# Kernel tuning notes

Hardware: AMD Instinct MI355X
Metric: run time of the kernel (lower is better)

The kernel has to match this reference:

```python
import jax, jax.numpy as jnp
import numpy as np

B, SX, SL, D, H = 4, 4096, 256, 1024, 16
DH = D // H
LN_EPS = 1e-5
RMS_EPS = 1e-8


def layernorm(x, g, b):
    mu = jnp.mean(x, axis=-1, keepdims=True)
    var = jnp.mean(jnp.square(x - mu), axis=-1, keepdims=True)
    return (x - mu) * jax.lax.rsqrt(var + LN_EPS) * g + b


def rmsnorm(x, gamma):
    # torch: norm = ||x||_2 * dim^-0.5 ; x / clamp(norm, eps) * gamma
    norm = jnp.sqrt(jnp.sum(jnp.square(x), axis=-1, keepdims=True)) * (DH ** -0.5)
    return x / jnp.maximum(norm, RMS_EPS) * gamma


def setup_inputs() -> dict:
    key = jax.random.key(0)
    ks = jax.random.split(key, 6)
    s = 0.02
    return {
        "x": jax.random.normal(ks[0], (B, SX, D), jnp.float32),
        "latents": jax.random.normal(ks[1], (B, SL, D), jnp.float32),
        "mask_x": jnp.ones((B, SX), jnp.float32),
        "mask_latent": jnp.ones((B, SL), jnp.float32),
        "ln_x_g": jnp.ones((D,), jnp.float32),
        "ln_x_b": jnp.zeros((D,), jnp.float32),
        "ln_l_g": jnp.ones((D,), jnp.float32),
        "ln_l_b": jnp.zeros((D,), jnp.float32),
        "Wq": jax.random.normal(ks[2], (D, D), jnp.float32) * s,
        "Wkv": jax.random.normal(ks[3], (D, 2 * D), jnp.float32) * s,
        "qk_gamma": jnp.ones((DH,), jnp.float32),
        "Wo": jax.random.normal(ks[4], (D, D), jnp.float32) * s,
    }


def reference(x, latents, mask_x, mask_latent, ln_x_g, ln_x_b, ln_l_g, ln_l_b, Wq, Wkv, qk_gamma, Wo):
    xn = layernorm(x, ln_x_g, ln_x_b)                       # [B,SX,D]
    ln = layernorm(latents, ln_l_g, ln_l_b)                 # [B,SL,D]

    q = (ln @ Wq).reshape(B, SL, H, DH).transpose(0, 2, 1, 3)      # [B,H,SL,DH]
    kv_in = jnp.concatenate([xn, ln], axis=1)                      # [B,SX+SL,D]
    kv = kv_in @ Wkv
    Skv = SX + SL
    k = kv[..., :D].reshape(B, Skv, H, DH).transpose(0, 2, 1, 3)   # [B,H,Skv,DH]
    v = kv[..., D:].reshape(B, Skv, H, DH).transpose(0, 2, 1, 3)

    # NOTE: original code applies query_norm to BOTH q and k (faithful to source)
    q = rmsnorm(q, qk_gamma)
    k = rmsnorm(k, qk_gamma)

    scores = jnp.einsum("bhqd,bhkd->bhqk", q, k) / np.sqrt(DH)     # [B,H,SL,Skv]

    kv_mask = jnp.concatenate([mask_x, mask_latent], axis=1)       # [B,Skv]
    mask = kv_mask[:, None, :] * mask_latent[:, :, None]           # [B,SL,Skv]
    add_mask = (1.0 - mask)[:, None, :, :] * jnp.finfo(scores.dtype).min
    attn = jax.nn.softmax(scores + add_mask, axis=-1)

    y = jnp.einsum("bhqk,bhkd->bhqd", attn, v)                     # [B,H,SL,DH]
    y = y.transpose(0, 2, 1, 3).reshape(B, SL, D)
    return y @ Wo
```

## Files before the change

### kernel.cpp

```cpp
#include <hip/hip_runtime.h>

#define NB   4
#define SXX  4096
#define SLL  256
#define DD   1024
#define HH   16
#define DHH  64
#define SKV  4352
#define MKV  17408
#define NSPLIT 8

typedef __attribute__((ext_vector_type(8))) short bfrag;
typedef __attribute__((ext_vector_type(4))) float facc;

__device__ __forceinline__ unsigned short f2bf(float f){
  unsigned u = __builtin_bit_cast(unsigned, f);
  u = (u + 0x7fffu + ((u >> 16) & 1u)) >> 16;
  return (unsigned short)u;
}
__device__ __forceinline__ float bf2f(unsigned short h){
  unsigned u = ((unsigned)h) << 16;
  return __builtin_bit_cast(float, u);
}

#define GLOAD_LDS16(g, lds) __builtin_amdgcn_global_load_lds( \
    (const __attribute__((address_space(1))) unsigned int*)(const void*)(g), \
    (__attribute__((address_space(3))) unsigned int*)(void*)(lds), 16, 0, 0)

__global__ void wtrans3(const float* __restrict__ Wq, const float* __restrict__ Wkv,
                        const float* __restrict__ Wo, unsigned short* __restrict__ wqt,
                        unsigned short* __restrict__ wkvt, unsigned short* __restrict__ wot){
  __shared__ float t[32][33];
  int z = blockIdx.z;
  const float* in; unsigned short* out; int N;
  if (z == 0){ in = Wq;  out = wqt;  N = DD;   }
  else if (z == 1){ in = Wkv; out = wkvt; N = 2*DD; }
  else { in = Wo;  out = wot;  N = DD;   }
  int n0 = blockIdx.x * 32, k0 = blockIdx.y * 32;
  if (n0 >= N) return;
  int tx = threadIdx.x, ty = threadIdx.y;
  #pragma unroll
  for (int i = 0; i < 4; i++)
    t[ty + 8*i][tx] = in[(size_t)(k0 + ty + 8*i) * N + n0 + tx];
  __syncthreads();
  #pragma unroll
  for (int i = 0; i < 4; i++)
    out[(size_t)(n0 + ty + 8*i) * DD + k0 + tx] = f2bf(t[tx][ty + 8*i]);
}

__global__ void lnorm(const float* __restrict__ src, const float* __restrict__ g,
                      const float* __restrict__ bt, unsigned short* __restrict__ kvin,
                      unsigned short* __restrict__ dst2, int seq, int off){
  int row = blockIdx.x;
  int b = row / seq, s = row - b*seq;
  int t = threadIdx.x;
  const float4* rp = (const float4*)(src + (size_t)row * DD);
  float4 v = rp[t];
  float sum = v.x + v.y + v.z + v.w;
  float sq  = v.x*v.x + v.y*v.y + v.z*v.z + v.w*v.w;
  #pragma unroll
  for (int o = 32; o > 0; o >>= 1){ sum += __shfl_down(sum, o); sq += __shfl_down(sq, o); }
  __shared__ float ls[8];
  int w = t >> 6, l = t & 63;
  if (l == 0){ ls[w] = sum; ls[4 + w] = sq; }
  __syncthreads();
  sum = ls[0] + ls[1] + ls[2] + ls[3];
  sq  = ls[4] + ls[5] + ls[6] + ls[7];
  float mu  = sum * (1.f/DD);
  float var = sq * (1.f/DD) - mu*mu;
  float rs  = rsqrtf(var + 1e-5f);
  float4 gv = ((const float4*)g)[t];
  float4 bv = ((const float4*)bt)[t];
  ushort4 o4;
  o4.x = f2bf((v.x - mu)*rs*gv.x + bv.x);
  o4.y = f2bf((v.y - mu)*rs*gv.y + bv.y);
  o4.z = f2bf((v.z - mu)*rs*gv.z + bv.z);
  o4.w = f2bf((v.w - mu)*rs*gv.w + bv.w);
  *(ushort4*)(kvin + (size_t)(b*SKV + off + s) * DD + t*4) = o4;
  if (dst2) *(ushort4*)(dst2 + (size_t)row * DD + t*4) = o4;
}

__global__ __launch_bounds__(256) void gemm64(const unsigned short* __restrict__ A,
    const unsigned short* __restrict__ Bt, int M, int N, int K, float* __restrict__ outF){
  __shared__ unsigned short lA[64][72];
  __shared__ unsigned short lB[64][72];
  int n0 = blockIdx.x * 64, m0 = blockIdx.y * 64;
  int t = threadIdx.x, w = t >> 6, l = t & 63;
  int wr = (w >> 1) * 32, wc = (w & 1) * 32;
  int lr = l & 15, kq = (l >> 4) * 8;
  facc acc00 = (facc)0.f, acc01 = (facc)0.f, acc10 = (facc)0.f, acc11 = (facc)0.f;
  for (int k0 = 0; k0 < K; k0 += 64){
    #pragma unroll
    for (int cc = 0; cc < 2; cc++){
      int ch = t + cc*256;
      int row = ch >> 3, cg = (ch & 7) * 8;
      *(bfrag*)&lA[row][cg] = *(const bfrag*)&A[(size_t)(m0 + row) * K + k0 + cg];
      *(bfrag*)&lB[row][cg] = *(const bfrag*)&Bt[(size_t)(n0 + row) * K + k0 + cg];
    }
    __syncthreads();
    #pragma unroll
    for (int ks = 0; ks < 2; ks++){
      bfrag a0 = *(const bfrag*)&lA[wr + lr][ks*32 + kq];
      bfrag a1 = *(const bfrag*)&lA[wr + 16 + lr][ks*32 + kq];
      bfrag b0 = *(const bfrag*)&lB[wc + lr][ks*32 + kq];
      bfrag b1 = *(const bfrag*)&lB[wc + 16 + lr][ks*32 + kq];
      acc00 = __builtin_amdgcn_mfma_f32_16x16x32_bf16(a0, b0, acc00, 0, 0, 0);
      acc01 = __builtin_amdgcn_mfma_f32_16x16x32_bf16(a0, b1, acc01, 0, 0, 0);
      acc10 = __builtin_amdgcn_mfma_f32_16x16x32_bf16(a1, b0, acc10, 0, 0, 0);
      acc11 = __builtin_amdgcn_mfma_f32_16x16x32_bf16(a1, b1, acc11, 0, 0, 0);
    }
    __syncthreads();
  }
  int rl = (l >> 4) * 4, cl = l & 15;
  facc accs[2][2] = {{acc00, acc01},{acc10, acc11}};
  #pragma unroll
  for (int mt = 0; mt < 2; mt++)
  #pragma unroll
  for (int nt = 0; nt < 2; nt++)
  #pragma unroll
  for (int j = 0; j < 4; j++){
    int r = m0 + wr + mt*16 + rl + j;
    int c = n0 + wc + nt*16 + cl;
    outF[(size_t)r * N + c] = accs[mt][nt][j];
  }
}

__global__ __launch_bounds__(256) void gemm_q(const unsigned short* __restrict__ A,
    const unsigned short* __restrict__ Bt, const float* __restrict__ gamma,
    unsigned short* __restrict__ qn){
  __shared__ char smemb[18432];
  unsigned short* lA = (unsigned short*)smemb;
  unsigned short* lB = lA + 64*72;
  float* Cf = (float*)smemb;
  int h = blockIdx.x, n0 = h * 64, m0 = blockIdx.y * 64;
  int t = threadIdx.x, w = t >> 6, l = t & 63;
  int wr = (w >> 1) * 32, wc = (w & 1) * 32;
  int lr = l & 15, kq = (l >> 4) * 8;
  facc acc00 = (facc)0.f, acc01 = (facc)0.f, acc10 = (facc)0.f, acc11 = (facc)0.f;
  for (int k0 = 0; k0 < 1024; k0 += 64){
    #pragma unroll
    for (int cc = 0; cc < 2; cc++){
      int ch = t + cc*256;
      int row = ch >> 3, cg = (ch & 7) * 8;
      *(bfrag*)&lA[row*72 + cg] = *(const bfrag*)&A[(size_t)(m0 + row) * 1024 + k0 + cg];
      *(bfrag*)&lB[row*72 + cg] = *(const bfrag*)&Bt[(size_t)(n0 + row) * 1024 + k0 + cg];
    }
    __syncthreads();
    #pragma unroll
    for (int ks = 0; ks < 2; ks++){
      bfrag a0 = *(const bfrag*)&lA[(wr + lr)*72 + ks*32 + kq];
      bfrag a1 = *(const bfrag*)&lA[(wr + 16 + lr)*72 + ks*32 + kq];
      bfrag b0 = *(const bfrag*)&lB[(wc + lr)*72 + ks*32 + kq];
      bfrag b1 = *(const bfrag*)&lB[(wc + 16 + lr)*72 + ks*32 + kq];
      acc00 = __builtin_amdgcn_mfma_f32_16x16x32_bf16(a0, b0, acc00, 0, 0, 0);
      acc01 = __builtin_amdgcn_mfma_f32_16x16x32_bf16(a0, b1, acc01, 0, 0, 0);
      acc10 = __builtin_amdgcn_mfma_f32_16x16x32_bf16(a1, b0, acc10, 0, 0, 0);
      acc11 = __builtin_amdgcn_mfma_f32_16x16x32_bf16(a1, b1, acc11, 0, 0, 0);
    }
    __syncthreads();
  }
  int rl = (l >> 4) * 4, cl = l & 15;
  facc accs[2][2] = {{acc00, acc01},{acc10, acc11}};
  #pragma unroll
  for (int mt = 0; mt < 2; mt++)
  #pragma unroll
  for (int nt = 0; nt < 2; nt++)
  #pragma unroll
  for (int j = 0; j < 4; j++)
    Cf[(wr + mt*16 + rl + j)*66 + wc + nt*16 + cl] = accs[mt][nt][j];
  __syncthreads();
  if (t < 64){
    const float* src = &Cf[t*66];
    float ss = 0.f;
    #pragma unroll
    for (int d = 0; d < 64; d++){ float a = src[d]; ss = fmaf(a, a, ss); }
    float rv = 0.125f / fmaxf(sqrtf(ss) * 0.125f, 1e-8f);
    int r = m0 + t, b = r >> 8, sl = r & 255;
    unsigned short* dst = &qn[((size_t)(b*HH + h)*SLL + sl)*DHH];
    #pragma unroll
    for (int i = 0; i < 8; i++){
      ushort4 p; float g;
      g = gamma[i*8+0]; p.x = f2bf(src[i*8+0]*g*g*rv);
      g = gamma[i*8+1]; p.y = f2bf(src[i*8+1]*g*g*rv);
      g = gamma[i*8+2]; p.z = f2bf(src[i*8+2]*g*g*rv);
      g = gamma[i*8+3]; p.w = f2bf(src[i*8+3]*g*g*rv);
      ushort4 q;
      g = gamma[i*8+4]; q.x = f2bf(src[i*8+4]*g*g*rv);
      g = gamma[i*8+5]; q.y = f2bf(src[i*8+5]*g*g*rv);
      g = gamma[i*8+6]; q.z = f2bf(src[i*8+6]*g*g*rv);
      g = gamma[i*8+7]; q.w = f2bf(src[i*8+7]*g*g*rv);
      *(ushort4*)&dst[i*8]     = p;
      *(ushort4*)&dst[i*8 + 4] = q;
    }
  }
}

__global__ __launch_bounds__(512, 2) void gemm_kv(const unsigned short* __restrict__ A,
    const unsigned short* __restrict__ Bt,
    const float* __restrict__ mask_x, const float* __restrict__ mask_lat,
    unsigned short* __restrict__ outK, unsigned short* __restrict__ outV,
    float* __restrict__ rkm){
  __shared__ alignas(16) unsigned short lds[3 * 24576];
  int bid = blockIdx.x;
  int wg = (bid & 7) * 136 + (bid >> 3);
  int m0 = (wg >> 4) * 256, n0 = (wg & 15) * 128;
  int t = threadIdx.x, w = t >> 6, l = t & 63;
  int wm = w >> 1, wn = w & 1;
  int lr = l & 15, q2 = l >> 4;
  int r8 = l >> 3, u = l & 7;
  int swz = (u ^ (r8 & 7)) * 8;
  const unsigned short* Ag = A  + (size_t)(m0 + w*8 + r8) * 1024 + swz;
  const unsigned short* Bg = Bt + (size_t)(n0 + w*8 + r8) * 1024 + swz;

  facc acc[4][4];
  #pragma unroll
  for (int mt = 0; mt < 4; mt++)
  #pragma unroll
  for (int nt = 0; nt < 4; nt++) acc[mt][nt] = (facc)0.f;

#define SBAR __builtin_amdgcn_sched_barrier(0)
#define KV_BARRIER do { SBAR; __builtin_amdgcn_s_barrier(); SBAR; } while(0)
#define KV_STA(j, i) GLOAD_LDS16(Ag + (size_t)(i)*65536 + (j)*64, \
    &lds[((j) % 3)*24576 + (i)*4096 + w*512])
#define KV_STB(j, i) GLOAD_LDS16(Bg + (size_t)(i)*65536 + (j)*64, \
    &lds[((j) % 3)*24576 + 16384 + (i)*4096 + w*512])
#define KV_LDF(va, vb, j, ks) { \
    const unsigned short* pA = &lds[((j) % 3)*24576 + (wm*64 + lr)*64 + (((ks)*4 + q2) ^ (lr & 7))*8]; \
    const unsigned short* pB = &lds[((j) % 3)*24576 + 16384 + (wn*64 + lr)*64 + (((ks)*4 + q2) ^ (lr & 7))*8]; \
    va[0] = *(const bfrag*)(pA);        va[1] = *(const bfrag*)(pA + 1024); \
    va[2] = *(const bfrag*)(pA + 2048); va[3] = *(const bfrag*)(pA + 3072); \
    vb[0] = *(const bfrag*)(pB);        vb[1] = *(const bfrag*)(pB + 1024); \
    vb[2] = *(const bfrag*)(pB + 2048); vb[3] = *(const bfrag*)(pB + 3072); }
#define KV_MFMA(va, vb) do { \
    __builtin_amdgcn_s_setprio(1); \
    _Pragma("unroll") \
    for (int mt = 0; mt < 4; mt++){ \
      _Pragma("unroll") \
      for (int nt = 0; nt < 4; nt++) \
        acc[mt][nt] = __builtin_amdgcn_mfma_f32_16x16x32_bf16(va[mt], vb[nt], acc[mt][nt], 0, 0, 0); } \
    __builtin_amdgcn_s_setprio(0); } while(0)

  KV_STA(0,0); KV_STA(0,1); KV_STA(0,2); KV_STA(0,3); KV_STB(0,0); KV_STB(0,1);
  KV_STA(1,0); KV_STA(1,1); KV_STA(1,2); KV_STA(1,3); KV_STB(1,0); KV_STB(1,1);
  __asm__ volatile("s_waitcnt vmcnt(6)" ::: "memory");
  KV_BARRIER;

  bfrag av[4], bv[4];
  #pragma unroll
  for (int j = 0; j < 16; j++){
    KV_LDF(av, bv, j, 0);
    if (j < 14){ KV_STA(j+2, 0); KV_STA(j+2, 1); KV_STB(j+2, 0); }
    KV_MFMA(av, bv);
    KV_LDF(av, bv, j, 1);
    if (j < 14){ KV_STA(j+2, 2); KV_STA(j+2, 3); KV_STB(j+2, 1); }
    KV_MFMA(av, bv);
    if (j < 14)       { __asm__ volatile("s_waitcnt vmcnt(6)" ::: "memory"); }
    else if (j == 14) { __asm__ volatile("s_waitcnt vmcnt(0)" ::: "memory"); }
    KV_BARRIER;
  }
#undef KV_STA
#undef KV_STB
#undef KV_LDF
#undef KV_MFMA

  int b = m0 / SKV, s0 = m0 - b*SKV;
  if (n0 < DD){
    #pragma unroll
    for (int mt = 0; mt < 4; mt++)
    #pragma unroll
    for (int nt = 0; nt < 4; nt++)
    #pragma unroll
    for (int j = 0; j < 4; j++)
      lds[(wm*64 + mt*16 + q2*4 + j)*136 + wn*64 + nt*16 + lr] = f2bf(acc[mt][nt][j]);
    __syncthreads();
    int s = t >> 1, hf = t & 1;
    int srow = s0 + s;
    float cm = (srow < SXX) ? mask_x[b*SXX + srow] : mask_lat[b*SLL + srow - SXX];
    const unsigned short* src = &lds[s*136 + hf*64];
    uint4 wv[8];
    #pragma unroll
    for (int i = 0; i < 8; i++) wv[i] = *(const uint4*)&src[i*8];
    float ss0 = 0.f, ss1 = 0.f;
    #pragma unroll
    for (int i = 0; i < 8; i++){
      const unsigned short* pp = (const unsigned short*)&wv[i];
      #pragma unroll
      for (int e = 0; e < 4; e++){
        float a = bf2f(pp[e]);     ss0 = fmaf(a, a, ss0);
        float c = bf2f(pp[e + 4]); ss1 = fmaf(c, c, ss1);
      }
    }
    float rv = 1.f / fmaxf(sqrtf(ss0 + ss1) * 0.125f, 1e-8f);
    int h = (n0 >> 6) + hf;
    unsigned short* dst = &outK[((size_t)(b*HH + h)*SKV + srow)*DHH];
    #pragma unroll
    for (int i = 0; i < 8; i++)
      *(uint4*)&dst[i*8] = wv[i];
    rkm[((size_t)(b*HH + h))*SKV + srow] = (cm != 0.f) ? rv : -1.f;
  } else {
    #pragma unroll
    for (int mt = 0; mt < 4; mt++)
    #pragma unroll
    for (int nt = 0; nt < 4; nt++){
      ushort4 p;
      p.x = f2bf(acc[mt][nt][0]); p.y = f2bf(acc[mt][nt][1]);
      p.z = f2bf(acc[mt][nt][2]); p.w = f2bf(acc[mt][nt][3]);
      *(ushort4*)&lds[(wn*64 + nt*16 + lr)*264 + wm*64 + mt*16 + q2*4] = p;
    }
    __syncthreads();
    int c = t >> 2, sq = t & 3;
    int hh = ((n0 - DD) >> 6) + (c >> 6), d = c & 63;
    const unsigned short* src = &lds[c*264 + sq*64];
    unsigned short* dst = &outV[((size_t)(b*HH + hh)*DHH + d)*SKV + s0 + sq*64];
    #pragma unroll
    for (int i = 0; i < 8; i++)
      *(uint4*)&dst[i*8] = *(const uint4*)&src[i*8];
  }
}

__global__ __launch_bounds__(256) void attn(const unsigned short* __restrict__ qn,
    const unsigned short* __restrict__ kbuf, const unsigned short* __restrict__ vT,
    const float* __restrict__ rkm, const float* __restrict__ mask_lat,
    float* __restrict__ Opart, float* __restrict__ lpart){
  int bh = blockIdx.y, split = blockIdx.z;
  int b = bh >> 4;
  __shared__ unsigned short lP[4][4][16][68];
  int t = threadIdx.x, w = t >> 6, l = t & 63;
  int lr = l & 15, q2 = l >> 4, kq = q2 * 8;
  bfrag aq0[4], aq1[4];
  float rm[4][4];
  #pragma unroll
  for (int tt = 0; tt < 4; tt++){
    const unsigned short* qbase = qn + ((size_t)bh * SLL + tt*64 + w*16 + lr) * DHH;
    aq0[tt] = *(const bfrag*)&qbase[kq];
    aq1[tt] = *(const bfrag*)&qbase[32 + kq];
    #pragma unroll
    for (int j = 0; j < 4; j++) rm[tt][j] = mask_lat[b*SLL + tt*64 + w*16 + q2*4 + j];
  }
  facc O[4][4];
  #pragma unroll
  for (int tt = 0; tt < 4; tt++)
  #pragma unroll
  for (int nt = 0; nt < 4; nt++) O[tt][nt] = (facc)0.f;
  float lsum[4][4];
  #pragma unroll
  for (int tt = 0; tt < 4; tt++)
  #pragma unroll
  for (int j = 0; j < 4; j++) lsum[tt][j] = 0.f;

  int t0 = (split * 68) / NSPLIT, t1 = ((split + 1) * 68) / NSPLIT;
  for (int kt = t0; kt < t1; kt++){
    int key0 = kt * 64;
    const unsigned short* kb = kbuf + ((size_t)bh * SKV + key0) * DHH;
    bfrag bk0[4], bk1[4]; float rk[4];
    #pragma unroll
    for (int nt = 0; nt < 4; nt++){
      bk0[nt] = *(const bfrag*)&kb[(nt*16 + lr)*DHH + kq];
      bk1[nt] = *(const bfrag*)&kb[(nt*16 + lr)*DHH + 32 + kq];
      rk[nt]  = rkm[(size_t)bh*SKV + key0 + nt*16 + lr];
    }
    const unsigned short* vb = vT + (size_t)bh * DHH * SKV + key0;
    bfrag bv0[4], bv1[4];
    #pragma unroll
    for (int nt = 0; nt < 4; nt++){
      bv0[nt] = *(const bfrag*)&vb[(size_t)(nt*16 + lr)*SKV + kq];
      bv1[nt] = *(const bfrag*)&vb[(size_t)(nt*16 + lr)*SKV + 32 + kq];
    }
    #pragma unroll
    for (int tt = 0; tt < 4; tt++){
      facc S[4];
      #pragma unroll
      for (int nt = 0; nt < 4; nt++){
        S[nt] = (facc)0.f;
        S[nt] = __builtin_amdgcn_mfma_f32_16x16x32_bf16(aq0[tt], bk0[nt], S[nt], 0, 0, 0);
        S[nt] = __builtin_amdgcn_mfma_f32_16x16x32_bf16(aq1[tt], bk1[nt], S[nt], 0, 0, 0);
      }
      #pragma unroll
      for (int j = 0; j < 4; j++){
        float rs_ = 0.f;
        #pragma unroll
        for (int nt = 0; nt < 4; nt++){
          float x = S[nt][j] * rk[nt];
          float sv = (rk[nt] >= 0.f && rm[tt][j] != 0.f) ? x : -3.0e38f;
          float p = __expf(sv - 8.0f);
          rs_ += p;
          lP[w][tt][q2*4 + j][nt*16 + lr] = f2bf(p);
        }
        lsum[tt][j] += rs_;
      }
    }
    __asm__ volatile("s_waitcnt lgkmcnt(0)" ::: "memory");
    #pragma unroll
    for (int tt = 0; tt < 4; tt++){
      bfrag ap0 = *(const bfrag*)&lP[w][tt][lr][kq];
      bfrag ap1 = *(const bfrag*)&lP[w][tt][lr][32 + kq];
      #pragma unroll
      for (int nt = 0; nt < 4; nt++){
        O[tt][nt] = __builtin_amdgcn_mfma_f32_16x16x32_bf16(ap0, bv0[nt], O[tt][nt], 0, 0, 0);
        O[tt][nt] = __builtin_amdgcn_mfma_f32_16x16x32_bf16(ap1, bv1[nt], O[tt][nt], 0, 0, 0);
      }
    }
  }
  #pragma unroll
  for (int tt = 0; tt < 4; tt++)
  #pragma unroll
  for (int j = 0; j < 4; j++){
    float L = lsum[tt][j];
    L += __shfl_xor(L, 1); L += __shfl_xor(L, 2);
    L += __shfl_xor(L, 4); L += __shfl_xor(L, 8);
    int srow = tt*64 + w*16 + q2*4 + j;
    size_t obase = (((size_t)split*64 + bh)*SLL + srow)*DHH;
    #pragma unroll
    for (int nt = 0; nt < 4; nt++)
      Opart[obase + nt*16 + lr] = O[tt][nt][j];
    if (lr == 0)
      lpart[((size_t)split*64 + bh)*SLL + srow] = L;
  }
}

__global__ __launch_bounds__(256) void attn_combine(const float* __restrict__ Opart,
    const float* __restrict__ lpart, unsigned short* __restrict__ ybuf){
  int t = threadIdx.x, w = t >> 6, l = t & 63;
  int idx = blockIdx.x * 4 + w;
  int bh = idx >> 8, srow = idx & 255;
  int b = bh >> 4, h = bh & 15;
  float L = 0.f, acc = 0.f;
  #pragma unroll
  for (int s = 0; s < NSPLIT; s++){
    L   += lpart[((size_t)s*64 + bh)*SLL + srow];
    acc += Opart[(((size_t)s*64 + bh)*SLL + srow)*DHH + l];
  }
  ybuf[((size_t)b*SLL + srow)*DD + h*DHH + l] = f2bf(acc / L);
}

extern "C" void kernel_launch(void* const* d_in, const int* in_sizes, int n_in,
                              void* d_out, int out_size, void* d_ws, size_t ws_size,
                              hipStream_t stream) {
  const float* x        = (const float*)d_in[0];
  const float* latents  = (const float*)d_in[1];
  const float* mask_x   = (const float*)d_in[2];
  const float* mask_lat = (const float*)d_in[3];
  const float* ln_x_g   = (const float*)d_in[4];
  const float* ln_x_b   = (const float*)d_in[5];
  const float* ln_l_g   = (const float*)d_in[6];
  const float* ln_l_b   = (const float*)d_in[7];
  const float* Wq       = (const float*)d_in[8];
  const float* Wkv      = (const float*)d_in[9];
  const float* qk_gamma = (const float*)d_in[10];
  const float* Wo       = (const float*)d_in[11];
  float* out = (float*)d_out;

  char* wsb = (char*)d_ws;
  unsigned short* kvin  = (unsigned short*)(wsb + 0);
  unsigned short* lnlat = (unsigned short*)(wsb + 35651584);
  unsigned short* wqt   = (unsigned short*)(wsb + 37748736);
  unsigned short* wkvt  = (unsigned short*)(wsb + 39845888);
  unsigned short* wot   = (unsigned short*)(wsb + 44040192);
  unsigned short* qnb   = (unsigned short*)(wsb + 50331648);
  unsigned short* kbuf  = (unsigned short*)(wsb + 52428800);
  unsigned short* vT    = (unsigned short*)(wsb + 88080384);
  float*          rkm   = (float*)(wsb + 123731968);
  unsigned short* ybuf  = (unsigned short*)(wsb + 124846080);
  float*          Opart = (float*)(wsb + 0);
  float*          lpart = (float*)(wsb + 35651584);

  wtrans3<<<dim3(64, 32, 3), dim3(32, 8), 0, stream>>>(Wq, Wkv, Wo, wqt, wkvt, wot);

  lnorm<<<NB*SXX, 256, 0, stream>>>(x,       ln_x_g, ln_x_b, kvin, nullptr, SXX, 0);
  lnorm<<<NB*SLL, 256, 0, stream>>>(latents, ln_l_g, ln_l_b, kvin, lnlat,   SLL, SXX);

  gemm_q<<<dim3(16, 16), 256, 0, stream>>>(lnlat, wqt, qk_gamma, qnb);
  gemm_kv<<<dim3(1088), 512, 0, stream>>>(kvin, wkvt, mask_x, mask_lat, kbuf, vT, rkm);

  attn<<<dim3(1, NB*HH, NSPLIT), 256, 0, stream>>>(qnb, kbuf, vT, rkm, mask_lat, Opart, lpart);
  attn_combine<<<(NB*HH*SLL)/4, 256, 0, stream>>>(Opart, lpart, ybuf);

  gemm64<<<dim3(DD/64, (NB*SLL)/64), 256, 0, stream>>>(ybuf, wot, NB*SLL, DD, DD, out);
}
```

Baseline: 354.5 us.

## Enlarge KV GEMM tile to 256x256 with double-buffered quarter-step pipeline

Reworks the K/V projection GEMM so each 512-thread workgroup computes a 256x256 output tile instead of 256x128, halving the grid to 544 blocks. Each wave now holds 8x4 accumulators. LDS staging moves from a triple buffer to a 64K-element double buffer, with loads split into half-tiles interleaved across four barrier-separated MFMA phases per k-step. The epilogue writes K/V in two 128-column chunks through LDS. The larger tile raises operand reuse and cuts global traffic, but it uses more registers and LDS (likely one block per CU), adds more barriers, and leaves fewer workgroups to fill the GPU.

```diff
diff --git a/kernel.cpp b/kernel.cpp
--- a/kernel.cpp
+++ b/kernel.cpp
@@ -200,121 +200,152 @@
     const float* __restrict__ mask_x, const float* __restrict__ mask_lat,
     unsigned short* __restrict__ outK, unsigned short* __restrict__ outV,
     float* __restrict__ rkm){
-  __shared__ alignas(16) unsigned short lds[3 * 24576];
+  __shared__ alignas(16) unsigned short lds[65536];
   int bid = blockIdx.x;
-  int wg = (bid & 7) * 136 + (bid >> 3);
-  int m0 = (wg >> 4) * 256, n0 = (wg & 15) * 128;
+  int wg = (bid & 7) * 68 + (bid >> 3);
+  int m0 = (wg >> 3) * 256, n0 = (wg & 7) * 256;
   int t = threadIdx.x, w = t >> 6, l = t & 63;
-  int wm = w >> 1, wn = w & 1;
+  int wm = w >> 2, wn = w & 3;
   int lr = l & 15, q2 = l >> 4;
   int r8 = l >> 3, u = l & 7;
-  int swz = (u ^ (r8 & 7)) * 8;
+  int swz = (u ^ r8) * 8;
   const unsigned short* Ag = A  + (size_t)(m0 + w*8 + r8) * 1024 + swz;
   const unsigned short* Bg = Bt + (size_t)(n0 + w*8 + r8) * 1024 + swz;
 
-  facc acc[4][4];
-  #pragma unroll
-  for (int mt = 0; mt < 4; mt++)
+  facc acc[8][4];
+  #pragma unroll
+  for (int mt = 0; mt < 8; mt++)
   #pragma unroll
   for (int nt = 0; nt < 4; nt++) acc[mt][nt] = (facc)0.f;
 
 #define SBAR __builtin_amdgcn_sched_barrier(0)
-#define KV_BARRIER do { SBAR; __builtin_amdgcn_s_barrier(); SBAR; } while(0)
-#define KV_STA(j, i) GLOAD_LDS16(Ag + (size_t)(i)*65536 + (j)*64, \
-    &lds[((j) % 3)*24576 + (i)*4096 + w*512])
-#define KV_STB(j, i) GLOAD_LDS16(Bg + (size_t)(i)*65536 + (j)*64, \
-    &lds[((j) % 3)*24576 + 16384 + (i)*4096 + w*512])
-#define KV_LDF(va, vb, j, ks) { \
-    const unsigned short* pA = &lds[((j) % 3)*24576 + (wm*64 + lr)*64 + (((ks)*4 + q2) ^ (lr & 7))*8]; \
-    const unsigned short* pB = &lds[((j) % 3)*24576 + 16384 + (wn*64 + lr)*64 + (((ks)*4 + q2) ^ (lr & 7))*8]; \
-    va[0] = *(const bfrag*)(pA);        va[1] = *(const bfrag*)(pA + 1024); \
-    va[2] = *(const bfrag*)(pA + 2048); va[3] = *(const bfrag*)(pA + 3072); \
-    vb[0] = *(const bfrag*)(pB);        vb[1] = *(const bfrag*)(pB + 1024); \
-    vb[2] = *(const bfrag*)(pB + 2048); vb[3] = *(const bfrag*)(pB + 3072); }
-#define KV_MFMA(va, vb) do { \
+#define BAR  __builtin_amdgcn_s_barrier()
+#define ST_A(tj, h, sw) GLOAD_LDS16(Ag + (size_t)((h)*128 + (sw)*64)*1024 + (tj)*64, \
+    &lds[((tj)&1)*32768 + ((h)*128 + (sw)*64 + w*8)*64])
+#define ST_B(tj, h, sw) GLOAD_LDS16(Bg + (size_t)((h)*128 + (sw)*64)*1024 + (tj)*64, \
+    &lds[((tj)&1)*32768 + 16384 + ((h)*128 + (sw)*64 + w*8)*64])
+#define ST_AH(tj, h) do{ ST_A(tj, h, 0); ST_A(tj, h, 1); }while(0)
+#define ST_BH(tj, h) do{ ST_B(tj, h, 0); ST_B(tj, h, 1); }while(0)
+#define LDF(tj, mh, ks) { \
+    int cs = (((ks)*4 + q2) ^ (lr & 7)) * 8; \
+    const unsigned short* pA = &lds[((tj)&1)*32768 + ((mh)*128 + wm*16 + lr)*64 + cs]; \
+    const unsigned short* pB = &lds[((tj)&1)*32768 + 16384 + (wn*16 + lr)*64 + cs]; \
+    av[0] = *(const bfrag*)(pA);        av[1] = *(const bfrag*)(pA + 2048); \
+    av[2] = *(const bfrag*)(pA + 4096); av[3] = *(const bfrag*)(pA + 6144); \
+    bv[0] = *(const bfrag*)(pB);        bv[1] = *(const bfrag*)(pB + 4096); \
+    bv[2] = *(const bfrag*)(pB + 8192); bv[3] = *(const bfrag*)(pB + 12288); }
+#define MFMA_Q(mh) do { \
     __builtin_amdgcn_s_setprio(1); \
     _Pragma("unroll") \
-    for (int mt = 0; mt < 4; mt++){ \
+    for (int i = 0; i < 4; i++){ \
       _Pragma("unroll") \
       for (int nt = 0; nt < 4; nt++) \
-        acc[mt][nt] = __builtin_amdgcn_mfma_f32_16x16x32_bf16(va[mt], vb[nt], acc[mt][nt], 0, 0, 0); } \
+        acc[(mh)*4 + i][nt] = __builtin_amdgcn_mfma_f32_16x16x32_bf16(av[i], bv[nt], acc[(mh)*4 + i][nt], 0, 0, 0); } \
     __builtin_amdgcn_s_setprio(0); } while(0)
-
-  KV_STA(0,0); KV_STA(0,1); KV_STA(0,2); KV_STA(0,3); KV_STB(0,0); KV_STB(0,1);
-  KV_STA(1,0); KV_STA(1,1); KV_STA(1,2); KV_STA(1,3); KV_STB(1,0); KV_STB(1,1);
-  __asm__ volatile("s_waitcnt vmcnt(6)" ::: "memory");
-  KV_BARRIER;
+#define LGKM0 do{ __asm__ volatile("s_waitcnt lgkmcnt(0)" ::: "memory"); SBAR; }while(0)
+
+  ST_AH(0,0); ST_AH(0,1); ST_BH(0,0); ST_BH(0,1); ST_AH(1,0);
+  __asm__ volatile("s_waitcnt vmcnt(2)" ::: "memory");
+  BAR;
 
   bfrag av[4], bv[4];
   #pragma unroll
-  for (int j = 0; j < 16; j++){
-    KV_LDF(av, bv, j, 0);
-    if (j < 14){ KV_STA(j+2, 0); KV_STA(j+2, 1); KV_STB(j+2, 0); }
-    KV_MFMA(av, bv);
-    KV_LDF(av, bv, j, 1);
-    if (j < 14){ KV_STA(j+2, 2); KV_STA(j+2, 3); KV_STB(j+2, 1); }
-    KV_MFMA(av, bv);
-    if (j < 14)       { __asm__ volatile("s_waitcnt vmcnt(6)" ::: "memory"); }
-    else if (j == 14) { __asm__ volatile("s_waitcnt vmcnt(0)" ::: "memory"); }
-    KV_BARRIER;
-  }
-#undef KV_STA
-#undef KV_STB
-#undef KV_LDF
-#undef KV_MFMA
+  for (int tj = 0; tj < 16; tj++){
+    LDF(tj, 0, 0);
+    if (tj + 1 < 16) ST_AH(tj+1, 1);
+    BAR; LGKM0;
+    MFMA_Q(0);
+    BAR;
+    LDF(tj, 1, 0);
+    if (tj + 1 < 16) ST_BH(tj+1, 0);
+    BAR; LGKM0;
+    MFMA_Q(1);
+    BAR;
+    LDF(tj, 0, 1);
+    if (tj + 1 < 16) ST_BH(tj+1, 1);
+    BAR; LGKM0;
+    MFMA_Q(0);
+    BAR;
+    LDF(tj, 1, 1);
+    if (tj + 2 < 16) ST_AH(tj+2, 0);
+    BAR; LGKM0;
+    MFMA_Q(1);
+    if (tj <= 13)      { __asm__ volatile("s_waitcnt vmcnt(2)" ::: "memory"); }
+    else if (tj == 14) { __asm__ volatile("s_waitcnt vmcnt(0)" ::: "memory"); }
+    BAR;
+  }
+#undef ST_A
+#undef ST_B
+#undef ST_AH
+#undef ST_BH
+#undef LDF
+#undef MFMA_Q
+#undef LGKM0
 
   int b = m0 / SKV, s0 = m0 - b*SKV;
   if (n0 < DD){
     #pragma unroll
-    for (int mt = 0; mt < 4; mt++)
-    #pragma unroll
-    for (int nt = 0; nt < 4; nt++)
-    #pragma unroll
-    for (int j = 0; j < 4; j++)
-      lds[(wm*64 + mt*16 + q2*4 + j)*136 + wn*64 + nt*16 + lr] = f2bf(acc[mt][nt][j]);
-    __syncthreads();
-    int s = t >> 1, hf = t & 1;
-    int srow = s0 + s;
-    float cm = (srow < SXX) ? mask_x[b*SXX + srow] : mask_lat[b*SLL + srow - SXX];
-    const unsigned short* src = &lds[s*136 + hf*64];
-    uint4 wv[8];
-    #pragma unroll
-    for (int i = 0; i < 8; i++) wv[i] = *(const uint4*)&src[i*8];
-    float ss0 = 0.f, ss1 = 0.f;
-    #pragma unroll
-    for (int i = 0; i < 8; i++){
-      const unsigned short* pp = (const unsigned short*)&wv[i];
-      #pragma unroll
-      for (int e = 0; e < 4; e++){
-        float a = bf2f(pp[e]);     ss0 = fmaf(a, a, ss0);
-        float c = bf2f(pp[e + 4]); ss1 = fmaf(c, c, ss1);
+    for (int ch = 0; ch < 2; ch++){
+      if (ch) __syncthreads();
+      #pragma unroll
+      for (int mt = 0; mt < 8; mt++)
+      #pragma unroll
+      for (int k = 0; k < 2; k++){
+        int nt = ch*2 + k;
+        #pragma unroll
+        for (int j = 0; j < 4; j++)
+          lds[(mt*32 + wm*16 + q2*4 + j)*136 + k*64 + wn*16 + lr] = f2bf(acc[mt][nt][j]);
       }
-    }
-    float rv = 1.f / fmaxf(sqrtf(ss0 + ss1) * 0.125f, 1e-8f);
-    int h = (n0 >> 6) + hf;
-    unsigned short* dst = &outK[((size_t)(b*HH + h)*SKV + srow)*DHH];
-    #pragma unroll
-    for (int i = 0; i < 8; i++)
-      *(uint4*)&dst[i*8] = wv[i];
-    rkm[((size_t)(b*HH + h))*SKV + srow] = (cm != 0.f) ? rv : -1.f;
+      __syncthreads();
+      int s = t >> 1, hf = t & 1;
+      int srow = s0 + s;
+      float cm = (srow < SXX) ? mask_x[b*SXX + srow] : mask_lat[b*SLL + srow - SXX];
+      const unsigned short* src = &lds[s*136 + hf*64];
+      uint4 wv[8];
+      #pragma unroll
+      for (int i = 0; i < 8; i++) wv[i] = *(const uint4*)&src[i*8];
+      float ss0 = 0.f, ss1 = 0.f;
+      #pragma unroll
+      for (int i = 0; i < 8; i++){
+        const unsigned short* pp = (const unsigned short*)&wv[i];
+        #pragma unroll
+        for (int e = 0; e < 4; e++){
+          float a = bf2f(pp[e]);     ss0 = fmaf(a, a, ss0);
+          float c = bf2f(pp[e + 4]); ss1 = fmaf(c, c, ss1);
+        }
+      }
+      float rv = 1.f / fmaxf(sqrtf(ss0 + ss1) * 0.125f, 1e-8f);
+      int h = (n0 >> 6) + ch*2 + hf;
+      unsigned short* dst = &outK[((size_t)(b*HH + h)*SKV + srow)*DHH];
+      #pragma unroll
+      for (int i = 0; i < 8; i++)
+        *(uint4*)&dst[i*8] = wv[i];
+      rkm[((size_t)(b*HH + h))*SKV + srow] = (cm != 0.f) ? rv : -1.f;
+    }
   } else {
     #pragma unroll
-    for (int mt = 0; mt < 4; mt++)
-    #pragma unroll
-    for (int nt = 0; nt < 4; nt++){
-      ushort4 p;
-      p.x = f2bf(acc[mt][nt][0]); p.y = f2bf(acc[mt][nt][1]);
-      p.z = f2bf(acc[mt][nt][2]); p.w = f2bf(acc[mt][nt][3]);
-      *(ushort4*)&lds[(wn*64 + nt*16 + lr)*264 + wm*64 + mt*16 + q2*4] = p;
-    }
-    __syncthreads();
-    int c = t >> 2, sq = t & 3;
-    int hh = ((n0 - DD) >> 6) + (c >> 6), d = c & 63;
-    const unsigned short* src = &lds[c*264 + sq*64];
-    unsigned short* dst = &outV[((size_t)(b*HH + hh)*DHH + d)*SKV + s0 + sq*64];
-    #pragma unroll
-    for (int i = 0; i < 8; i++)
-      *(uint4*)&dst[i*8] = *(const uint4*)&src[i*8];
+    for (int ch = 0; ch < 2; ch++){
+      if (ch) __syncthreads();
+      #pragma unroll
+      for (int mt = 0; mt < 8; mt++)
+      #pragma unroll
+      for (int k = 0; k < 2; k++){
+        int nt = ch*2 + k;
+        ushort4 p;
+        p.x = f2bf(acc[mt][nt][0]); p.y = f2bf(acc[mt][nt][1]);
+        p.z = f2bf(acc[mt][nt][2]); p.w = f2bf(acc[mt][nt][3]);
+        *(ushort4*)&lds[(k*64 + wn*16 + lr)*264 + mt*32 + wm*16 + q2*4] = p;
+      }
+      __syncthreads();
+      int c = t >> 2, sq = t & 3;
+      int gcol = (n0 - DD) + ch*128 + c;
+      int hh = gcol >> 6, d = gcol & 63;
+      const unsigned short* src = &lds[c*264 + sq*64];
+      unsigned short* dst = &outV[((size_t)(b*HH + hh)*DHH + d)*SKV + s0 + sq*64];
+      #pragma unroll
+      for (int i = 0; i < 8; i++)
+        *(uint4*)&dst[i*8] = *(const uint4*)&src[i*8];
+    }
   }
 }
 
@@ -470,7 +501,7 @@
   lnorm<<<NB*SLL, 256, 0, stream>>>(latents, ln_l_g, ln_l_b, kvin, lnlat,   SLL, SXX);
 
   gemm_q<<<dim3(16, 16), 256, 0, stream>>>(lnlat, wqt, qk_gamma, qnb);
-  gemm_kv<<<dim3(1088), 512, 0, stream>>>(kvin, wkvt, mask_x, mask_lat, kbuf, vT, rkm);
+  gemm_kv<<<dim3(544), 512, 0, stream>>>(kvin, wkvt, mask_x, mask_lat, kbuf, vT, rkm);
 
   attn<<<dim3(1, NB*HH, NSPLIT), 256, 0, stream>>>(qnb, kbuf, vT, rkm, mask_lat, Opart, lpart);
   attn_combine<<<(NB*HH*SLL)/4, 256, 0, stream>>>(Opart, lpart, ybuf);
```

After: 352.3 us. About the same (-0.6%).
